# Kernel optimization log

Hardware: AMD Instinct MI355X
Metric: run time of the kernel (lower is better)

The kernel has to match this reference:

```python
import jax, jax.numpy as jnp
import numpy as np

N_NODES = 100000
DIM = 128
N_EDGES = 1600000
BN_EPS = 1e-5


def setup_inputs() -> dict:
    key = jax.random.key(0)
    ks = jax.random.split(key, 8)
    x = jax.random.normal(ks[0], (N_NODES, DIM), dtype=jnp.float32)
    ei = jax.random.randint(ks[1], (2, N_EDGES), 0, N_NODES, dtype=jnp.int32)
    # GINConv train_eps scalar
    eps = jnp.zeros((), dtype=jnp.float32)
    # MLP: Linear(dim, 2*dim) -> BN(2*dim) -> ReLU -> Dropout -> Linear(2*dim, dim) -> BN(dim) -> ReLU
    s1 = 1.0 / np.sqrt(DIM)
    s2 = 1.0 / np.sqrt(2 * DIM)
    W1 = jax.random.uniform(ks[2], (DIM, 2 * DIM), jnp.float32, -s1, s1)
    b1 = jax.random.uniform(ks[3], (2 * DIM,), jnp.float32, -s1, s1)
    W2 = jax.random.uniform(ks[4], (2 * DIM, DIM), jnp.float32, -s2, s2)
    b2 = jax.random.uniform(ks[5], (DIM,), jnp.float32, -s2, s2)
    g1 = jnp.ones((2 * DIM,), jnp.float32)
    be1 = jnp.zeros((2 * DIM,), jnp.float32)
    m1 = jax.random.normal(ks[6], (2 * DIM,), jnp.float32) * 0.1
    v1 = jnp.ones((2 * DIM,), jnp.float32)
    g2 = jnp.ones((DIM,), jnp.float32)
    be2 = jnp.zeros((DIM,), jnp.float32)
    m2 = jax.random.normal(ks[7], (DIM,), jnp.float32) * 0.1
    v2 = jnp.ones((DIM,), jnp.float32)
    return {"x": x, "eps": eps, "W1": W1, "b1": b1, "g1": g1, "be1": be1,
            "m1": m1, "v1": v1, "W2": W2, "b2": b2, "g2": g2, "be2": be2,
            "m2": m2, "v2": v2, "ei": ei}


def _bn(h, gamma, beta, mean, var):
    # BatchNorm1d in eval mode (running stats)
    return gamma * (h - mean) * jax.lax.rsqrt(var + BN_EPS) + beta


def reference(x, eps, W1, b1, g1, be1, m1, v1, W2, b2, g2, be2, m2, v2, ei):
    src, dst = ei[0], ei[1]
    # GIN aggregation: sum of neighbor (source) features scattered to destination
    agg = jax.ops.segment_sum(x[src], dst, num_segments=N_NODES)  # [N, dim]
    h = (1.0 + eps) * x + agg
    h = jax.nn.relu(_bn(h @ W1 + b1, g1, be1, m1, v1))  # [N, 2*dim]
    # Dropout is identity in eval mode
    h = jax.nn.relu(_bn(h @ W2 + b2, g2, be2, m2, v2))  # [N, dim]
    return h
```

## Files before the change

### kernel.cpp

```cpp
#include <hip/hip_runtime.h>

#define N_NODES 100000
#define DIM     128
#define HID     256
#define BN_EPS  1e-5f
#define TILES16 6250
#define MLP_GRID 512
#define BK_BITS 9
#define NBK     196
#define BKCAP   12288
#define EPB     4096
#define CVT_BLOCKS 3125

typedef _Float16     half8  __attribute__((ext_vector_type(8)));
typedef float        f32x4  __attribute__((ext_vector_type(4)));

static __device__ __forceinline__ f32x4 mfma16h(half8 a, half8 b, f32x4 c) {
    return __builtin_amdgcn_mfma_f32_16x16x32_f16(a, b, c, 0, 0, 0);
}

__global__ __launch_bounds__(256) void binscatter_kernel(
    const int* __restrict__ src, const int* __restrict__ dst,
    int* __restrict__ cursor, unsigned int* __restrict__ pairs, int nE) {
    __shared__ int cnt[NBK];
    __shared__ int gbase[NBK];
    int t = threadIdx.x;
    for (int i = t; i < NBK; i += 256) cnt[i] = 0;
    __syncthreads();
    int e0 = blockIdx.x * EPB;
    int n = min(EPB, nE - e0);
    int d[16];
#pragma unroll
    for (int k = 0; k < 16; ++k) {
        int idx = t + k * 256;
        if (idx < n) {
            d[k] = dst[e0 + idx];
            atomicAdd(&cnt[d[k] >> BK_BITS], 1);
        }
    }
    __syncthreads();
    for (int i = t; i < NBK; i += 256) {
        int c = cnt[i];
        gbase[i] = c ? atomicAdd(&cursor[i], c) : 0;
    }
    __syncthreads();
    for (int i = t; i < NBK; i += 256) cnt[i] = 0;
    __syncthreads();
#pragma unroll
    for (int k = 0; k < 16; ++k) {
        int idx = t + k * 256;
        if (idx < n) {
            int b = d[k] >> BK_BITS;
            int r = atomicAdd(&cnt[b], 1);
            pairs[(long long)b * BKCAP + gbase[b] + r] =
                ((unsigned)src[e0 + idx] << BK_BITS) | ((unsigned)d[k] & 511u);
        }
    }
}

__global__ __launch_bounds__(512) void fill_cvt_kernel(
    const unsigned int* __restrict__ pairs, const int* __restrict__ cursor,
    int* __restrict__ rowptr, int* __restrict__ csr_src,
    const float* __restrict__ x, _Float16* __restrict__ x16) {
    int t = threadIdx.x;
    if (blockIdx.x >= NBK) {
        int bc = blockIdx.x - NBK;
#pragma unroll
        for (int k = 0; k < 2; ++k) {
            int i = bc * 1024 + k * 512 + t;
            float4 v = ((const float4*)x)[i];
            _Float16 h0 = (_Float16)v.x, h1 = (_Float16)v.y,
                     h2 = (_Float16)v.z, h3 = (_Float16)v.w;
            unsigned long long pk =
                (unsigned long long)__builtin_bit_cast(unsigned short, h0)
              | ((unsigned long long)__builtin_bit_cast(unsigned short, h1) << 16)
              | ((unsigned long long)__builtin_bit_cast(unsigned short, h2) << 32)
              | ((unsigned long long)__builtin_bit_cast(unsigned short, h3) << 48);
            ((unsigned long long*)x16)[i] = pk;
        }
        return;
    }
    __shared__ int cnt[512];
    __shared__ int off[512];
    __shared__ int stmp[256];
    __shared__ int s_base;
    int b = blockIdx.x;
    if (t < 256) stmp[t] = (t < NBK) ? cursor[t] : 0;
    __syncthreads();
    for (int s = 1; s < 256; s <<= 1) {
        int a = (t >= s && t < 256) ? stmp[t - s] : 0;
        __syncthreads();
        if (t < 256) stmp[t] += a;
        __syncthreads();
    }
    if (t == 0) s_base = stmp[b] - cursor[b];
    __syncthreads();
    int base = s_base;
    int m = cursor[b];
    int nd0 = b << BK_BITS;
    int nn = min(512, N_NODES - nd0);
    const unsigned int* bp = pairs + (long long)b * BKCAP;
    cnt[t] = 0;
    __syncthreads();
    for (int e = t; e < m; e += 512)
        atomicAdd(&cnt[bp[e] & 511u], 1);
    __syncthreads();
    int v = cnt[t];
    off[t] = v;
    __syncthreads();
    for (int s = 1; s < 512; s <<= 1) {
        int a = (t >= s) ? off[t - s] : 0;
        __syncthreads();
        off[t] += a;
        __syncthreads();
    }
    int excl = off[t] - v;
    __syncthreads();
    off[t] = excl;
    if (t < nn) rowptr[nd0 + t] = base + excl;
    if (b == NBK - 1 && t == 0) rowptr[N_NODES] = base + m;
    cnt[t] = 0;
    __syncthreads();
    for (int e = t; e < m; e += 512) {
        unsigned int p = bp[e];
        int li = p & 511u;
        int r = atomicAdd(&cnt[li], 1);
        csr_src[base + off[li] + r] = (int)(p >> BK_BITS);
    }
}

__global__ __launch_bounds__(256) void gather_kernel(
    const _Float16* __restrict__ x16, const float* __restrict__ epsp,
    const int* __restrict__ rowptr, const int* __restrict__ csr_src,
    _Float16* __restrict__ h16) {
    int node = blockIdx.x * 4 + (threadIdx.x >> 6);
    int lane = threadIdx.x & 63;
    int g = lane >> 4;
    int part = lane & 15;
    const half8* xp = (const half8*)x16;
    int beg = rowptr[node], end = rowptr[node + 1];
    float s[8] = {0,0,0,0,0,0,0,0};
    int j = beg;
    for (; j + 8 <= end; j += 8) {
        int n0 = csr_src[j + g];
        int n1 = csr_src[j + 4 + g];
        half8 v0 = xp[n0 * 16 + part];
        half8 v1 = xp[n1 * 16 + part];
#pragma unroll
        for (int i = 0; i < 8; ++i) s[i] += (float)v0[i] + (float)v1[i];
    }
    int r = end - j;
    if (g < r) {
        half8 v = xp[csr_src[j + g] * 16 + part];
#pragma unroll
        for (int i = 0; i < 8; ++i) s[i] += (float)v[i];
    }
    if (g + 4 < r) {
        half8 v = xp[csr_src[j + 4 + g] * 16 + part];
#pragma unroll
        for (int i = 0; i < 8; ++i) s[i] += (float)v[i];
    }
#pragma unroll
    for (int i = 0; i < 8; ++i) {
        s[i] += __shfl_xor(s[i], 16);
        s[i] += __shfl_xor(s[i], 32);
    }
    if (lane < 16) {
        float sc = 1.f + epsp[0];
        half8 xv = xp[node * 16 + part];
        half8 o;
#pragma unroll
        for (int i = 0; i < 8; ++i) o[i] = (_Float16)fmaf(sc, (float)xv[i], s[i]);
        ((half8*)h16)[node * 16 + part] = o;
    }
}

__global__ __launch_bounds__(256, 2) void mlp_fused_kernel(
    const _Float16* __restrict__ h16,
    const float* __restrict__ W1, const float* __restrict__ b1,
    const float* __restrict__ g1, const float* __restrict__ be1,
    const float* __restrict__ m1, const float* __restrict__ v1,
    const float* __restrict__ W2, const float* __restrict__ b2,
    const float* __restrict__ g2, const float* __restrict__ be2,
    const float* __restrict__ m2, const float* __restrict__ v2,
    float* __restrict__ out) {
    __shared__ _Float16 sh1[16 * HID];
    int t = threadIdx.x;
    int cg = t >> 6, l = t & 63;
    int l15 = l & 15, q = l >> 4;

    half8 B1[4][4];
    float s1v[4], sh1v[4];
#pragma unroll
    for (int nt = 0; nt < 4; ++nt) {
        int col = 64 * cg + 16 * nt + l15;
#pragma unroll
        for (int ks = 0; ks < 4; ++ks) {
            half8 bh;
#pragma unroll
            for (int i = 0; i < 8; ++i)
                bh[i] = (_Float16)W1[(32 * ks + 8 * q + i) * HID + col];
            B1[nt][ks] = bh;
        }
        float sc = g1[col] * rsqrtf(v1[col] + BN_EPS);
        s1v[nt] = sc;
        sh1v[nt] = (b1[col] - m1[col]) * sc + be1[col];
    }
    half8 B2[2][8];
    float s2v[2], sh2v[2];
#pragma unroll
    for (int nt = 0; nt < 2; ++nt) {
        int col = 32 * cg + 16 * nt + l15;
#pragma unroll
        for (int ks = 0; ks < 8; ++ks) {
            half8 bh;
#pragma unroll
            for (int i = 0; i < 8; ++i)
                bh[i] = (_Float16)W2[(32 * ks + 8 * q + i) * DIM + col];
            B2[nt][ks] = bh;
        }
        float sc = g2[col] * rsqrtf(v2[col] + BN_EPS);
        s2v[nt] = sc;
        sh2v[nt] = (b2[col] - m2[col]) * sc + be2[col];
    }

    for (int tile = blockIdx.x; tile < TILES16; tile += MLP_GRID) {
        int row0 = tile * 16;
        const _Float16* arow = h16 + (long long)(row0 + l15) * DIM;
        half8 A[4];
#pragma unroll
        for (int ks = 0; ks < 4; ++ks) A[ks] = *(const half8*)(arow + 32 * ks + 8 * q);
        f32x4 acc[4];
#pragma unroll
        for (int nt = 0; nt < 4; ++nt) acc[nt] = (f32x4)(0.f);
#pragma unroll
        for (int nt = 0; nt < 4; ++nt)
#pragma unroll
            for (int ks = 0; ks < 4; ++ks)
                acc[nt] = mfma16h(A[ks], B1[nt][ks], acc[nt]);
#pragma unroll
        for (int nt = 0; nt < 4; ++nt) {
            int col = 64 * cg + 16 * nt + l15;
#pragma unroll
            for (int reg = 0; reg < 4; ++reg) {
                int row = 4 * q + reg;
                float vv = fmaxf(0.f, fmaf(acc[nt][reg], s1v[nt], sh1v[nt]));
                sh1[row * HID + (col ^ ((row & 7) << 3))] = (_Float16)vv;
            }
        }
        __syncthreads();
        half8 A2[8];
        {
            int row = l15;
            int sx = (row & 7) << 3;
#pragma unroll
            for (int ks = 0; ks < 8; ++ks)
                A2[ks] = *(const half8*)&sh1[row * HID + ((32 * ks + 8 * q) ^ sx)];
        }
        __syncthreads();
        f32x4 acc2[2];
        acc2[0] = (f32x4)(0.f); acc2[1] = (f32x4)(0.f);
#pragma unroll
        for (int nt = 0; nt < 2; ++nt)
#pragma unroll
            for (int ks = 0; ks < 8; ++ks)
                acc2[nt] = mfma16h(A2[ks], B2[nt][ks], acc2[nt]);
#pragma unroll
        for (int nt = 0; nt < 2; ++nt) {
            int col = 32 * cg + 16 * nt + l15;
#pragma unroll
            for (int reg = 0; reg < 4; ++reg) {
                int orow = row0 + 4 * q + reg;
                out[(long long)orow * DIM + col] =
                    fmaxf(0.f, fmaf(acc2[nt][reg], s2v[nt], sh2v[nt]));
            }
        }
    }
}

extern "C" void kernel_launch(void* const* d_in, const int* in_sizes, int n_in,
                              void* d_out, int out_size, void* d_ws, size_t ws_size,
                              hipStream_t stream) {
    const float* x   = (const float*)d_in[0];
    const float* eps = (const float*)d_in[1];
    const float* W1  = (const float*)d_in[2];
    const float* b1  = (const float*)d_in[3];
    const float* g1  = (const float*)d_in[4];
    const float* be1 = (const float*)d_in[5];
    const float* m1  = (const float*)d_in[6];
    const float* v1  = (const float*)d_in[7];
    const float* W2  = (const float*)d_in[8];
    const float* b2  = (const float*)d_in[9];
    const float* g2  = (const float*)d_in[10];
    const float* be2 = (const float*)d_in[11];
    const float* m2  = (const float*)d_in[12];
    const float* v2  = (const float*)d_in[13];
    const int*   ei  = (const int*)d_in[14];
    int nE = in_sizes[14] / 2;
    const int* src = ei;
    const int* dst = ei + nE;

    char* ws = (char*)d_ws;
    int*          cursor  = (int*)(ws + 0);
    int*          rowptr  = (int*)(ws + 4096);
    int*          csr_src = (int*)(ws + 405504);
    unsigned int* pairs   = (unsigned int*)(ws + 6806528);
    _Float16*     x16     = (_Float16*)(ws + 16441344);
    _Float16*     h16     = (_Float16*)(ws + 42041344);

    hipMemsetAsync(cursor, 0, NBK * sizeof(int), stream);
    binscatter_kernel<<<(nE + EPB - 1) / EPB, 256, 0, stream>>>(src, dst, cursor, pairs, nE);

    fill_cvt_kernel<<<NBK + CVT_BLOCKS, 512, 0, stream>>>(pairs, cursor, rowptr, csr_src,
                                                          x, x16);

    gather_kernel<<<N_NODES / 4, 256, 0, stream>>>(x16, eps, rowptr, csr_src, h16);

    mlp_fused_kernel<<<MLP_GRID, 256, 0, stream>>>(h16, W1, b1, g1, be1, m1, v1,
                                                   W2, b2, g2, be2, m2, v2, (float*)d_out);
}
```

Baseline: 149.6 us.

## Fuse neighbor gather with MLP and pre-transpose weights to fp16

Merges the gather kernel and the MLP kernel, so each 256-thread block aggregates 16 nodes into shared memory and runs both MFMA layers on them directly. This removes the h16 round trip through global memory and one kernel launch. Weights are converted to fp16 and transposed once in extra blocks of the fill kernel, and the fused kernel reads B fragments straight from global or L2 instead of holding them in registers. The cost is weight reads for every 16-node tile and a gather phase that may be unevenly loaded across the block's waves.

Measured after the change: 200.5 us. +34.0%, slower.

```diff
diff --git a/kernel.cpp b/kernel.cpp
--- a/kernel.cpp
+++ b/kernel.cpp
@@ -4,13 +4,12 @@
 #define DIM     128
 #define HID     256
 #define BN_EPS  1e-5f
-#define TILES16 6250
-#define MLP_GRID 512
 #define BK_BITS 9
 #define NBK     196
 #define BKCAP   12288
 #define EPB     4096
 #define CVT_BLOCKS 3125
+#define WPREP_BLOCKS 16
 
 typedef _Float16     half8  __attribute__((ext_vector_type(8)));
 typedef float        f32x4  __attribute__((ext_vector_type(4)));
@@ -61,8 +60,28 @@
 __global__ __launch_bounds__(512) void fill_cvt_kernel(
     const unsigned int* __restrict__ pairs, const int* __restrict__ cursor,
     int* __restrict__ rowptr, int* __restrict__ csr_src,
-    const float* __restrict__ x, _Float16* __restrict__ x16) {
+    const float* __restrict__ x, _Float16* __restrict__ x16,
+    const float* __restrict__ W1, const float* __restrict__ W2,
+    _Float16* __restrict__ W1T, _Float16* __restrict__ W2T) {
     int t = threadIdx.x;
+    if (blockIdx.x >= NBK + CVT_BLOCKS) {
+        int bc = blockIdx.x - NBK - CVT_BLOCKS;
+        int o0 = (bc & 7) * 4096 + t * 8;
+        if (bc < 8) {
+            int col = o0 >> 7, k0 = o0 & 127;
+            half8 v;
+#pragma unroll
+            for (int i = 0; i < 8; ++i) v[i] = (_Float16)W1[(k0 + i) * HID + col];
+            *(half8*)&W1T[o0] = v;
+        } else {
+            int col = o0 >> 8, k0 = o0 & 255;
+            half8 v;
+#pragma unroll
+            for (int i = 0; i < 8; ++i) v[i] = (_Float16)W2[(k0 + i) * DIM + col];
+            *(half8*)&W2T[o0] = v;
+        }
+        return;
+    }
     if (blockIdx.x >= NBK) {
         int bc = blockIdx.x - NBK;
 #pragma unroll
@@ -129,151 +148,124 @@
     }
 }
 
-__global__ __launch_bounds__(256) void gather_kernel(
+__global__ __launch_bounds__(256, 3) void gin_fused_kernel(
     const _Float16* __restrict__ x16, const float* __restrict__ epsp,
     const int* __restrict__ rowptr, const int* __restrict__ csr_src,
-    _Float16* __restrict__ h16) {
-    int node = blockIdx.x * 4 + (threadIdx.x >> 6);
-    int lane = threadIdx.x & 63;
-    int g = lane >> 4;
-    int part = lane & 15;
-    const half8* xp = (const half8*)x16;
-    int beg = rowptr[node], end = rowptr[node + 1];
-    float s[8] = {0,0,0,0,0,0,0,0};
-    int j = beg;
-    for (; j + 8 <= end; j += 8) {
-        int n0 = csr_src[j + g];
-        int n1 = csr_src[j + 4 + g];
-        half8 v0 = xp[n0 * 16 + part];
-        half8 v1 = xp[n1 * 16 + part];
-#pragma unroll
-        for (int i = 0; i < 8; ++i) s[i] += (float)v0[i] + (float)v1[i];
-    }
-    int r = end - j;
-    if (g < r) {
-        half8 v = xp[csr_src[j + g] * 16 + part];
-#pragma unroll
-        for (int i = 0; i < 8; ++i) s[i] += (float)v[i];
-    }
-    if (g + 4 < r) {
-        half8 v = xp[csr_src[j + 4 + g] * 16 + part];
-#pragma unroll
-        for (int i = 0; i < 8; ++i) s[i] += (float)v[i];
-    }
-#pragma unroll
-    for (int i = 0; i < 8; ++i) {
-        s[i] += __shfl_xor(s[i], 16);
-        s[i] += __shfl_xor(s[i], 32);
-    }
-    if (lane < 16) {
-        float sc = 1.f + epsp[0];
-        half8 xv = xp[node * 16 + part];
-        half8 o;
-#pragma unroll
-        for (int i = 0; i < 8; ++i) o[i] = (_Float16)fmaf(sc, (float)xv[i], s[i]);
-        ((half8*)h16)[node * 16 + part] = o;
-    }
-}
-
-__global__ __launch_bounds__(256, 2) void mlp_fused_kernel(
-    const _Float16* __restrict__ h16,
-    const float* __restrict__ W1, const float* __restrict__ b1,
-    const float* __restrict__ g1, const float* __restrict__ be1,
-    const float* __restrict__ m1, const float* __restrict__ v1,
-    const float* __restrict__ W2, const float* __restrict__ b2,
-    const float* __restrict__ g2, const float* __restrict__ be2,
-    const float* __restrict__ m2, const float* __restrict__ v2,
+    const _Float16* __restrict__ W1T, const _Float16* __restrict__ W2T,
+    const float* __restrict__ b1, const float* __restrict__ g1,
+    const float* __restrict__ be1, const float* __restrict__ m1,
+    const float* __restrict__ v1,
+    const float* __restrict__ b2, const float* __restrict__ g2,
+    const float* __restrict__ be2, const float* __restrict__ m2,
+    const float* __restrict__ v2,
     float* __restrict__ out) {
+    __shared__ _Float16 shh[16 * DIM];
     __shared__ _Float16 sh1[16 * HID];
     int t = threadIdx.x;
-    int cg = t >> 6, l = t & 63;
-    int l15 = l & 15, q = l >> 4;
-
-    half8 B1[4][4];
-    float s1v[4], sh1v[4];
+    int w = t >> 6, lane = t & 63;
+    int g = lane >> 4, part = lane & 15;
+    int node0 = blockIdx.x * 16;
+    const half8* xp = (const half8*)x16;
+    float sc = 1.f + epsp[0];
+
+    for (int it = 0; it < 4; ++it) {
+        int ln = 4 * w + it;
+        int node = node0 + ln;
+        int beg = rowptr[node], end = rowptr[node + 1];
+        float s[8] = {0,0,0,0,0,0,0,0};
+        int j = beg;
+        for (; j + 8 <= end; j += 8) {
+            int n0 = csr_src[j + g];
+            int n1 = csr_src[j + 4 + g];
+            half8 v0 = xp[n0 * 16 + part];
+            half8 v1 = xp[n1 * 16 + part];
+#pragma unroll
+            for (int i = 0; i < 8; ++i) s[i] += (float)v0[i] + (float)v1[i];
+        }
+        int r = end - j;
+        if (g < r) {
+            half8 v = xp[csr_src[j + g] * 16 + part];
+#pragma unroll
+            for (int i = 0; i < 8; ++i) s[i] += (float)v[i];
+        }
+        if (g + 4 < r) {
+            half8 v = xp[csr_src[j + 4 + g] * 16 + part];
+#pragma unroll
+            for (int i = 0; i < 8; ++i) s[i] += (float)v[i];
+        }
+#pragma unroll
+        for (int i = 0; i < 8; ++i) {
+            s[i] += __shfl_xor(s[i], 16);
+            s[i] += __shfl_xor(s[i], 32);
+        }
+        if (lane < 16) {
+            half8 xv = xp[node * 16 + part];
+            half8 o;
+#pragma unroll
+            for (int i = 0; i < 8; ++i) o[i] = (_Float16)fmaf(sc, (float)xv[i], s[i]);
+            *(half8*)&shh[ln * DIM + ((part * 8) ^ ((ln & 7) << 3))] = o;
+        }
+    }
+    __syncthreads();
+
+    int cg = w, l15 = lane & 15, q = lane >> 4;
+    half8 A[4];
+    {
+        int sx = (l15 & 7) << 3;
+#pragma unroll
+        for (int ks = 0; ks < 4; ++ks)
+            A[ks] = *(const half8*)&shh[l15 * DIM + ((32 * ks + 8 * q) ^ sx)];
+    }
+    f32x4 acc[4];
+#pragma unroll
+    for (int nt = 0; nt < 4; ++nt) acc[nt] = (f32x4)(0.f);
 #pragma unroll
     for (int nt = 0; nt < 4; ++nt) {
         int col = 64 * cg + 16 * nt + l15;
-#pragma unroll
-        for (int ks = 0; ks < 4; ++ks) {
-            half8 bh;
-#pragma unroll
-            for (int i = 0; i < 8; ++i)
-                bh[i] = (_Float16)W1[(32 * ks + 8 * q + i) * HID + col];
-            B1[nt][ks] = bh;
-        }
-        float sc = g1[col] * rsqrtf(v1[col] + BN_EPS);
-        s1v[nt] = sc;
-        sh1v[nt] = (b1[col] - m1[col]) * sc + be1[col];
-    }
-    half8 B2[2][8];
-    float s2v[2], sh2v[2];
+        const half8* bp = (const half8*)&W1T[col * DIM + 8 * q];
+#pragma unroll
+        for (int ks = 0; ks < 4; ++ks)
+            acc[nt] = mfma16h(A[ks], bp[ks * 4], acc[nt]);
+    }
+#pragma unroll
+    for (int nt = 0; nt < 4; ++nt) {
+        int col = 64 * cg + 16 * nt + l15;
+        float s1 = g1[col] * rsqrtf(v1[col] + BN_EPS);
+        float f1 = (b1[col] - m1[col]) * s1 + be1[col];
+#pragma unroll
+        for (int reg = 0; reg < 4; ++reg) {
+            int row = 4 * q + reg;
+            float vv = fmaxf(0.f, fmaf(acc[nt][reg], s1, f1));
+            sh1[row * HID + (col ^ ((row & 7) << 3))] = (_Float16)vv;
+        }
+    }
+    __syncthreads();
+    half8 A2[8];
+    {
+        int sx = (l15 & 7) << 3;
+#pragma unroll
+        for (int ks = 0; ks < 8; ++ks)
+            A2[ks] = *(const half8*)&sh1[l15 * HID + ((32 * ks + 8 * q) ^ sx)];
+    }
+    f32x4 acc2[2];
+    acc2[0] = (f32x4)(0.f); acc2[1] = (f32x4)(0.f);
 #pragma unroll
     for (int nt = 0; nt < 2; ++nt) {
         int col = 32 * cg + 16 * nt + l15;
-#pragma unroll
-        for (int ks = 0; ks < 8; ++ks) {
-            half8 bh;
-#pragma unroll
-            for (int i = 0; i < 8; ++i)
-                bh[i] = (_Float16)W2[(32 * ks + 8 * q + i) * DIM + col];
-            B2[nt][ks] = bh;
-        }
-        float sc = g2[col] * rsqrtf(v2[col] + BN_EPS);
-        s2v[nt] = sc;
-        sh2v[nt] = (b2[col] - m2[col]) * sc + be2[col];
-    }
-
-    for (int tile = blockIdx.x; tile < TILES16; tile += MLP_GRID) {
-        int row0 = tile * 16;
-        const _Float16* arow = h16 + (long long)(row0 + l15) * DIM;
-        half8 A[4];
-#pragma unroll
-        for (int ks = 0; ks < 4; ++ks) A[ks] = *(const half8*)(arow + 32 * ks + 8 * q);
-        f32x4 acc[4];
-#pragma unroll
-        for (int nt = 0; nt < 4; ++nt) acc[nt] = (f32x4)(0.f);
-#pragma unroll
-        for (int nt = 0; nt < 4; ++nt)
-#pragma unroll
-            for (int ks = 0; ks < 4; ++ks)
-                acc[nt] = mfma16h(A[ks], B1[nt][ks], acc[nt]);
-#pragma unroll
-        for (int nt = 0; nt < 4; ++nt) {
-            int col = 64 * cg + 16 * nt + l15;
-#pragma unroll
-            for (int reg = 0; reg < 4; ++reg) {
-                int row = 4 * q + reg;
-                float vv = fmaxf(0.f, fmaf(acc[nt][reg], s1v[nt], sh1v[nt]));
-                sh1[row * HID + (col ^ ((row & 7) << 3))] = (_Float16)vv;
-            }
-        }
-        __syncthreads();
-        half8 A2[8];
-        {
-            int row = l15;
-            int sx = (row & 7) << 3;
-#pragma unroll
-            for (int ks = 0; ks < 8; ++ks)
-                A2[ks] = *(const half8*)&sh1[row * HID + ((32 * ks + 8 * q) ^ sx)];
-        }
-        __syncthreads();
-        f32x4 acc2[2];
-        acc2[0] = (f32x4)(0.f); acc2[1] = (f32x4)(0.f);
-#pragma unroll
-        for (int nt = 0; nt < 2; ++nt)
-#pragma unroll
-            for (int ks = 0; ks < 8; ++ks)
-                acc2[nt] = mfma16h(A2[ks], B2[nt][ks], acc2[nt]);
-#pragma unroll
-        for (int nt = 0; nt < 2; ++nt) {
-            int col = 32 * cg + 16 * nt + l15;
-#pragma unroll
-            for (int reg = 0; reg < 4; ++reg) {
-                int orow = row0 + 4 * q + reg;
-                out[(long long)orow * DIM + col] =
-                    fmaxf(0.f, fmaf(acc2[nt][reg], s2v[nt], sh2v[nt]));
-            }
+        const half8* bp = (const half8*)&W2T[col * HID + 8 * q];
+#pragma unroll
+        for (int ks = 0; ks < 8; ++ks)
+            acc2[nt] = mfma16h(A2[ks], bp[ks * 4], acc2[nt]);
+    }
+#pragma unroll
+    for (int nt = 0; nt < 2; ++nt) {
+        int col = 32 * cg + 16 * nt + l15;
+        float s2 = g2[col] * rsqrtf(v2[col] + BN_EPS);
+        float f2 = (b2[col] - m2[col]) * s2 + be2[col];
+#pragma unroll
+        for (int reg = 0; reg < 4; ++reg) {
+            int orow = node0 + 4 * q + reg;
+            out[(long long)orow * DIM + col] = fmaxf(0.f, fmaf(acc2[nt][reg], s2, f2));
         }
     }
 }
@@ -306,16 +298,16 @@
     int*          csr_src = (int*)(ws + 405504);
     unsigned int* pairs   = (unsigned int*)(ws + 6806528);
     _Float16*     x16     = (_Float16*)(ws + 16441344);
-    _Float16*     h16     = (_Float16*)(ws + 42041344);
+    _Float16*     W1T     = (_Float16*)(ws + 42041344);
+    _Float16*     W2T     = (_Float16*)(ws + 42106880);
 
     hipMemsetAsync(cursor, 0, NBK * sizeof(int), stream);
     binscatter_kernel<<<(nE + EPB - 1) / EPB, 256, 0, stream>>>(src, dst, cursor, pairs, nE);
 
-    fill_cvt_kernel<<<NBK + CVT_BLOCKS, 512, 0, stream>>>(pairs, cursor, rowptr, csr_src,
-                                                          x, x16);
-
-    gather_kernel<<<N_NODES / 4, 256, 0, stream>>>(x16, eps, rowptr, csr_src, h16);
-
-    mlp_fused_kernel<<<MLP_GRID, 256, 0, stream>>>(h16, W1, b1, g1, be1, m1, v1,
-                                                   W2, b2, g2, be2, m2, v2, (float*)d_out);
-}
+    fill_cvt_kernel<<<NBK + CVT_BLOCKS + WPREP_BLOCKS, 512, 0, stream>>>(
+        pairs, cursor, rowptr, csr_src, x, x16, W1, W2, W1T, W2T);
+
+    gin_fused_kernel<<<N_NODES / 16, 256, 0, stream>>>(
+        x16, eps, rowptr, csr_src, W1T, W2T,
+        b1, g1, be1, m1, v1, b2, g2, be2, m2, v2, (float*)d_out);
+}
```

## Pre-transpose weights to fp16 once, double MLP grid, shrink binscatter blocks

Applied to the files above, without the earlier changes.

Adds 16 extra blocks to the fill/convert kernel that convert W1 and W2 to fp16 in a transposed, k-contiguous layout. Each MLP block can then load its B fragments with vector half8 loads instead of eight strided fp32 loads and conversions. The MLP grid is doubled so that prologue cost is spread over more resident blocks. Binscatter now handles half as many edges per block, with a smaller bucket capacity, which risks overflow if a bucket receives an unusually large share of edges.

Result: slower. 162.3 us (+8.5%).

```diff
diff --git a/kernel.cpp b/kernel.cpp
--- a/kernel.cpp
+++ b/kernel.cpp
@@ -5,12 +5,13 @@
 #define HID     256
 #define BN_EPS  1e-5f
 #define TILES16 6250
-#define MLP_GRID 512
+#define MLP_GRID 1024
 #define BK_BITS 9
 #define NBK     196
-#define BKCAP   12288
-#define EPB     4096
+#define BKCAP   11264
+#define EPB     2048
 #define CVT_BLOCKS 3125
+#define WPREP_BLOCKS 16
 
 typedef _Float16     half8  __attribute__((ext_vector_type(8)));
 typedef float        f32x4  __attribute__((ext_vector_type(4)));
@@ -29,9 +30,9 @@
     __syncthreads();
     int e0 = blockIdx.x * EPB;
     int n = min(EPB, nE - e0);
-    int d[16];
-#pragma unroll
-    for (int k = 0; k < 16; ++k) {
+    int d[8];
+#pragma unroll
+    for (int k = 0; k < 8; ++k) {
         int idx = t + k * 256;
         if (idx < n) {
             d[k] = dst[e0 + idx];
@@ -47,7 +48,7 @@
     for (int i = t; i < NBK; i += 256) cnt[i] = 0;
     __syncthreads();
 #pragma unroll
-    for (int k = 0; k < 16; ++k) {
+    for (int k = 0; k < 8; ++k) {
         int idx = t + k * 256;
         if (idx < n) {
             int b = d[k] >> BK_BITS;
@@ -61,8 +62,28 @@
 __global__ __launch_bounds__(512) void fill_cvt_kernel(
     const unsigned int* __restrict__ pairs, const int* __restrict__ cursor,
     int* __restrict__ rowptr, int* __restrict__ csr_src,
-    const float* __restrict__ x, _Float16* __restrict__ x16) {
+    const float* __restrict__ x, _Float16* __restrict__ x16,
+    const float* __restrict__ W1, const float* __restrict__ W2,
+    _Float16* __restrict__ W1T, _Float16* __restrict__ W2T) {
     int t = threadIdx.x;
+    if (blockIdx.x >= NBK + CVT_BLOCKS) {
+        int bc = blockIdx.x - NBK - CVT_BLOCKS;
+        int o0 = (bc & 7) * 4096 + t * 8;
+        if (bc < 8) {
+            int col = o0 >> 7, k0 = o0 & 127;
+            half8 v;
+#pragma unroll
+            for (int i = 0; i < 8; ++i) v[i] = (_Float16)W1[(k0 + i) * HID + col];
+            *(half8*)&W1T[o0] = v;
+        } else {
+            int col = o0 >> 8, k0 = o0 & 255;
+            half8 v;
+#pragma unroll
+            for (int i = 0; i < 8; ++i) v[i] = (_Float16)W2[(k0 + i) * DIM + col];
+            *(half8*)&W2T[o0] = v;
+        }
+        return;
+    }
     if (blockIdx.x >= NBK) {
         int bc = blockIdx.x - NBK;
 #pragma unroll
@@ -177,12 +198,13 @@
 
 __global__ __launch_bounds__(256, 2) void mlp_fused_kernel(
     const _Float16* __restrict__ h16,
-    const float* __restrict__ W1, const float* __restrict__ b1,
-    const float* __restrict__ g1, const float* __restrict__ be1,
-    const float* __restrict__ m1, const float* __restrict__ v1,
-    const float* __restrict__ W2, const float* __restrict__ b2,
-    const float* __restrict__ g2, const float* __restrict__ be2,
-    const float* __restrict__ m2, const float* __restrict__ v2,
+    const _Float16* __restrict__ W1T, const _Float16* __restrict__ W2T,
+    const float* __restrict__ b1, const float* __restrict__ g1,
+    const float* __restrict__ be1, const float* __restrict__ m1,
+    const float* __restrict__ v1,
+    const float* __restrict__ b2, const float* __restrict__ g2,
+    const float* __restrict__ be2, const float* __restrict__ m2,
+    const float* __restrict__ v2,
     float* __restrict__ out) {
     __shared__ _Float16 sh1[16 * HID];
     int t = threadIdx.x;
@@ -195,13 +217,8 @@
     for (int nt = 0; nt < 4; ++nt) {
         int col = 64 * cg + 16 * nt + l15;
 #pragma unroll
-        for (int ks = 0; ks < 4; ++ks) {
-            half8 bh;
-#pragma unroll
-            for (int i = 0; i < 8; ++i)
-                bh[i] = (_Float16)W1[(32 * ks + 8 * q + i) * HID + col];
-            B1[nt][ks] = bh;
-        }
+        for (int ks = 0; ks < 4; ++ks)
+            B1[nt][ks] = *(const half8*)&W1T[col * DIM + 32 * ks + 8 * q];
         float sc = g1[col] * rsqrtf(v1[col] + BN_EPS);
         s1v[nt] = sc;
         sh1v[nt] = (b1[col] - m1[col]) * sc + be1[col];
@@ -212,13 +229,8 @@
     for (int nt = 0; nt < 2; ++nt) {
         int col = 32 * cg + 16 * nt + l15;
 #pragma unroll
-        for (int ks = 0; ks < 8; ++ks) {
-            half8 bh;
-#pragma unroll
-            for (int i = 0; i < 8; ++i)
-                bh[i] = (_Float16)W2[(32 * ks + 8 * q + i) * DIM + col];
-            B2[nt][ks] = bh;
-        }
+        for (int ks = 0; ks < 8; ++ks)
+            B2[nt][ks] = *(const half8*)&W2T[col * HID + 32 * ks + 8 * q];
         float sc = g2[col] * rsqrtf(v2[col] + BN_EPS);
         s2v[nt] = sc;
         sh2v[nt] = (b2[col] - m2[col]) * sc + be2[col];
@@ -305,17 +317,20 @@
     int*          rowptr  = (int*)(ws + 4096);
     int*          csr_src = (int*)(ws + 405504);
     unsigned int* pairs   = (unsigned int*)(ws + 6806528);
-    _Float16*     x16     = (_Float16*)(ws + 16441344);
-    _Float16*     h16     = (_Float16*)(ws + 42041344);
+    _Float16*     x16     = (_Float16*)(ws + 15638528);
+    _Float16*     W1T     = (_Float16*)(ws + 41238528);
+    _Float16*     W2T     = (_Float16*)(ws + 41304064);
+    _Float16*     h16     = (_Float16*)(ws + 41369600);
 
     hipMemsetAsync(cursor, 0, NBK * sizeof(int), stream);
     binscatter_kernel<<<(nE + EPB - 1) / EPB, 256, 0, stream>>>(src, dst, cursor, pairs, nE);
 
-    fill_cvt_kernel<<<NBK + CVT_BLOCKS, 512, 0, stream>>>(pairs, cursor, rowptr, csr_src,
-                                                          x, x16);
+    fill_cvt_kernel<<<NBK + CVT_BLOCKS + WPREP_BLOCKS, 512, 0, stream>>>(
+        pairs, cursor, rowptr, csr_src, x, x16, W1, W2, W1T, W2T);
 
     gather_kernel<<<N_NODES / 4, 256, 0, stream>>>(x16, eps, rowptr, csr_src, h16);
 
-    mlp_fused_kernel<<<MLP_GRID, 256, 0, stream>>>(h16, W1, b1, g1, be1, m1, v1,
-                                                   W2, b2, g2, be2, m2, v2, (float*)d_out);
-}
+    mlp_fused_kernel<<<MLP_GRID, 256, 0, stream>>>(h16, W1T, W2T,
+                                                   b1, g1, be1, m1, v1,
+                                                   b2, g2, be2, m2, v2, (float*)d_out);
+}
```
